# Kernel optimization log

Hardware: AMD Instinct MI355X
Metric: run time of the kernel (lower is better)

The kernel has to match this reference:

```python
import jax, jax.numpy as jnp
import numpy as np

B, T, E, H, O = 64, 512, 512, 512, 512

def setup_inputs() -> dict:
    key = jax.random.key(0)
    k1, k2, k3, k4, k5 = jax.random.split(key, 5)
    s1 = 1.0 / np.sqrt(E + H)
    s2 = 1.0 / np.sqrt(H)
    return {
        "x": jax.random.normal(k1, (B, T, E), dtype=jnp.float32),
        "W1": jax.random.uniform(k2, (H, E + H), dtype=jnp.float32, minval=-s1, maxval=s1),
        "b1": jax.random.uniform(k3, (H,), dtype=jnp.float32, minval=-s1, maxval=s1),
        "W2": jax.random.uniform(k4, (O, H), dtype=jnp.float32, minval=-s2, maxval=s2),
        "b2": jax.random.uniform(k5, (O,), dtype=jnp.float32, minval=-s2, maxval=s2),
    }

def reference(x, W1, b1, W2, b2):
    b = x.shape[0]
    h0 = jnp.zeros((b, x.shape[2]), dtype=x.dtype)

    def step(hidden, xt):
        inp = jnp.concatenate([xt, hidden], axis=1)          # [b, e+h]
        hidden = jax.nn.relu(inp @ W1.T + b1)                # [b, h]
        out = hidden @ W2.T + b2                             # [b, o]
        return hidden, out

    # scan over time: x -> [t, b, e]
    h_final, outs = jax.lax.scan(step, h0, jnp.swapaxes(x, 0, 1))
    return jnp.swapaxes(outs, 0, 1), h_final
```

## Files before the change

kernel.cpp:

```cpp
#include <hip/hip_runtime.h>
#include <cstddef>
#include <type_traits>

#define T_STEPS 512
#define BATCH   64
#define EDIM    512
#define HDIM    512
#define ODIM    512

#define W_ELEMS  (32 * 4 * 64 * 8)
#define HB_ELEMS (16 * 512)

typedef __bf16 bf16;
typedef __bf16 bf16x4 __attribute__((ext_vector_type(4)));
typedef __bf16 bf16x8 __attribute__((ext_vector_type(8)));
typedef float  f32x4  __attribute__((ext_vector_type(4)));

__device__ __forceinline__ void barrier_lds() {
  asm volatile("s_waitcnt lgkmcnt(0)\n\ts_barrier" ::: "memory");
  __builtin_amdgcn_sched_barrier(0);
}

__device__ __forceinline__ void gload_lds16(const bf16* g, bf16* l) {
  __builtin_amdgcn_global_load_lds(
      (const __attribute__((address_space(1))) unsigned int*)g,
      (__attribute__((address_space(3))) unsigned int*)l, 16, 0, 0);
}

__global__ __launch_bounds__(256) void conv_f32_bf16_kernel(
    const float* __restrict__ src, bf16* __restrict__ dst,
    int srow_stride, int drow_elems)
{
  size_t i = ((size_t)blockIdx.x * 256 + threadIdx.x) * 8;
  size_t row = i / drow_elems, col = i % drow_elems;
  const float* s = src + row * srow_stride + col;
  f32x4 a = *(const f32x4*)s;
  f32x4 b = *(const f32x4*)(s + 4);
  bf16x8 v;
#pragma unroll
  for (int u = 0; u < 4; ++u) { v[u] = (bf16)a[u]; v[u + 4] = (bf16)b[u]; }
  *(bf16x8*)(dst + i) = v;
}

template <typename XT, bool REMAP>
__global__ __launch_bounds__(256) void gemm_mfma_kernel(
    const XT* __restrict__ X, int ldx,
    const float* __restrict__ W, int ldw, int kw0,
    const float* __restrict__ bias,
    float* __restrict__ C, int ldc, int K)
{
  __shared__ __align__(16) bf16 Asm[8 * 64 * 8];
  __shared__ __align__(16) bf16 Bsm[8 * 64 * 8];

  const int tid  = threadIdx.x;
  const int row0 = blockIdx.x * 128;
  const int col0 = blockIdx.y * 128;
  const int w    = tid >> 6, lane = tid & 63;
  const int q    = lane >> 4, nl = lane & 15;
  const int wm   = w >> 1, wn = w & 1;

  const int srow = tid >> 2;
  const int sq   = tid & 3;
  f32x4 acc[4][4] = {};

  for (int k0 = 0; k0 < K; k0 += 32) {
#pragma unroll
    for (int rep = 0; rep < 2; ++rep) {
      int rl = srow + rep * 64;
      int mt = rl >> 4, snl = rl & 15;
      bf16x8 v;
      const XT* src = X + (size_t)(row0 + rl) * ldx + k0 + sq * 8;
      if constexpr (std::is_same_v<XT, float>) {
        f32x4 a0 = *(const f32x4*)src;
        f32x4 a1 = *(const f32x4*)(src + 4);
#pragma unroll
        for (int u = 0; u < 4; ++u) { v[u] = (bf16)a0[u]; v[u + 4] = (bf16)a1[u]; }
      } else {
        v = *(const bf16x8*)src;
      }
      *(bf16x8*)&Asm[(size_t)((mt * 4 + sq) * 16 + snl) * 8] = v;
    }
#pragma unroll
    for (int rep = 0; rep < 2; ++rep) {
      int rl = srow + rep * 64;
      int nt = rl >> 4, snl = rl & 15;
      const float* src = W + (size_t)(col0 + rl) * ldw + kw0 + k0 + sq * 8;
      f32x4 b0 = *(const f32x4*)src;
      f32x4 b1 = *(const f32x4*)(src + 4);
      bf16x8 v;
#pragma unroll
      for (int u = 0; u < 4; ++u) { v[u] = (bf16)b0[u]; v[u + 4] = (bf16)b1[u]; }
      *(bf16x8*)&Bsm[(size_t)((nt * 4 + sq) * 16 + snl) * 8] = v;
    }
    __syncthreads();

    bf16x8 a[4], b[4];
#pragma unroll
    for (int i = 0; i < 4; ++i)
      a[i] = *(bf16x8*)&Asm[(size_t)((wm * 4 + i) * 64 + lane) * 8];
#pragma unroll
    for (int j = 0; j < 4; ++j)
      b[j] = *(bf16x8*)&Bsm[(size_t)((wn * 4 + j) * 64 + lane) * 8];
#pragma unroll
    for (int i = 0; i < 4; ++i)
#pragma unroll
      for (int j = 0; j < 4; ++j)
        acc[i][j] = __builtin_amdgcn_mfma_f32_16x16x32_bf16(a[i], b[j], acc[i][j], 0, 0, 0);
    __syncthreads();
  }

#pragma unroll
  for (int i = 0; i < 4; ++i)
#pragma unroll
    for (int j = 0; j < 4; ++j) {
      int colg = col0 + wn * 64 + j * 16 + nl;
#pragma unroll
      for (int r = 0; r < 4; ++r) {
        size_t rowg = (size_t)(row0 + wm * 64 + i * 16 + q * 4 + r);
        size_t crow = REMAP ? (((rowg & (T_STEPS - 1)) << 6) | (rowg >> 9)) : rowg;
        C[crow * ldc + colg] = acc[i][j][r] + bias[colg];
      }
    }
}

template <bool REMAP>
__global__ __launch_bounds__(256) void gemm_lds_kernel(
    const bf16* __restrict__ Abf, int lda,
    const bf16* __restrict__ Bbf, int ldb,
    const float* __restrict__ bias,
    float* __restrict__ C, int ldc, int K)
{
  __shared__ __align__(16) bf16 Asm[8 * 64 * 8];
  __shared__ __align__(16) bf16 Bsm[8 * 64 * 8];

  const int tid  = threadIdx.x;
  const int row0 = blockIdx.x * 128;
  const int col0 = blockIdx.y * 128;
  const int w    = tid >> 6, lane = tid & 63;
  const int q    = lane >> 4, nl = lane & 15;
  const int wm   = w >> 1, wn = w & 1;

  f32x4 acc[4][4] = {};

  for (int k0 = 0; k0 < K; k0 += 32) {
#pragma unroll
    for (int rep = 0; rep < 2; ++rep) {
      int idx = tid + rep * 256;
      int mt = idx >> 6, sq = (idx >> 4) & 3, snl = idx & 15;
      const bf16* ga = Abf + (size_t)(row0 + mt * 16 + snl) * lda + k0 + sq * 8;
      gload_lds16(ga, Asm + (size_t)(rep * 4 + w) * 512);
      const bf16* gb = Bbf + (size_t)(col0 + mt * 16 + snl) * ldb + k0 + sq * 8;
      gload_lds16(gb, Bsm + (size_t)(rep * 4 + w) * 512);
    }
    __syncthreads();

    bf16x8 a[4], b[4];
#pragma unroll
    for (int i = 0; i < 4; ++i)
      a[i] = *(bf16x8*)&Asm[(size_t)((wm * 4 + i) * 64 + lane) * 8];
#pragma unroll
    for (int j = 0; j < 4; ++j)
      b[j] = *(bf16x8*)&Bsm[(size_t)((wn * 4 + j) * 64 + lane) * 8];
#pragma unroll
    for (int i = 0; i < 4; ++i)
#pragma unroll
      for (int j = 0; j < 4; ++j)
        acc[i][j] = __builtin_amdgcn_mfma_f32_16x16x32_bf16(a[i], b[j], acc[i][j], 0, 0, 0);
    __syncthreads();
  }

#pragma unroll
  for (int i = 0; i < 4; ++i)
#pragma unroll
    for (int j = 0; j < 4; ++j) {
      int colg = col0 + wn * 64 + j * 16 + nl;
#pragma unroll
      for (int r = 0; r < 4; ++r) {
        size_t rowg = (size_t)(row0 + wm * 64 + i * 16 + q * 4 + r);
        size_t crow = REMAP ? (((rowg & (T_STEPS - 1)) << 6) | (rowg >> 9)) : rowg;
        C[crow * ldc + colg] = acc[i][j][r] + bias[colg];
      }
    }
}

template <int DBUF>
__global__ __launch_bounds__(512, 2) void scan_kernel(
    const float* __restrict__ A,
    const float* __restrict__ W1,
    bf16* __restrict__ Hbf)
{
  extern __shared__ __align__(16) bf16 smem[];
  bf16* Wlds = smem;
  bf16* hb0  = smem + W_ELEMS;
  bf16* hb1  = DBUF ? (hb0 + HB_ELEMS) : hb0;

  const int tid  = threadIdx.x;
  const int c    = blockIdx.x;
  const int w    = tid >> 6, lane = tid & 63;
  const int q    = lane >> 4, nl = lane & 15;
  const int rb0  = c * 16;
  const int n0   = w * 64;
  const int sw   = (nl & 7) << 3;

  for (int idx = tid; idx < 32 * 4 * 64; idx += 512) {
    int l  = idx & 63;
    int kt = (idx >> 6) & 3;
    int tg = idx >> 8;
    int n  = tg * 16 + (l & 15);
    int k  = kt * 32 + (l >> 4) * 8;
    const float* src = W1 + (size_t)n * (EDIM + HDIM) + EDIM + k;
    bf16x8 v;
#pragma unroll
    for (int u = 0; u < 8; ++u) v[u] = (bf16)src[u];
    *(bf16x8*)&Wlds[(size_t)idx * 8] = v;
  }

  bf16x8 Wreg[4][12];
#pragma unroll
  for (int i = 0; i < 4; ++i) {
    int n = n0 + i * 16 + nl;
    const float* wrow = W1 + (size_t)n * (EDIM + HDIM) + EDIM;
#pragma unroll
    for (int kt2 = 0; kt2 < 12; ++kt2) {
      const float* src = wrow + (kt2 + 4) * 32 + q * 8;
      bf16x8 v;
#pragma unroll
      for (int u = 0; u < 8; ++u) v[u] = (bf16)src[u];
      Wreg[i][kt2] = v;
    }
  }
  __syncthreads();

  f32x4 An[4];
  {
    const float* ap = A + (size_t)(rb0 + nl) * HDIM + n0 + q * 4;
    An[0] = *(const f32x4*)(ap);
    An[1] = *(const f32x4*)(ap + 16);
    An[2] = *(const f32x4*)(ap + 32);
    An[3] = *(const f32x4*)(ap + 48);
  }

  f32x4 acc[4];

  for (int t = 0; t < T_STEPS; ++t) {
    bf16* hr = (t & 1) ? hb1 : hb0;
    bf16* hw = (t & 1) ? hb0 : hb1;

#pragma unroll
    for (int i = 0; i < 4; ++i) acc[i] = An[i];
    {
      int tn = (t + 1 < T_STEPS) ? t + 1 : 0;
      const float* ap = A + ((size_t)tn * BATCH + rb0 + nl) * HDIM + n0 + q * 4;
      An[0] = *(const f32x4*)(ap);
      An[1] = *(const f32x4*)(ap + 16);
      An[2] = *(const f32x4*)(ap + 32);
      An[3] = *(const f32x4*)(ap + 48);
    }

    if (t > 0) {
#pragma unroll
      for (int kt = 0; kt < 16; ++kt) {
        bf16x8 af = *(bf16x8*)&hr[nl * 512 + ((kt * 32 + q * 8) ^ sw)];
        if (kt < 4) {
#pragma unroll
          for (int i = 0; i < 4; ++i) {
            bf16x8 wb = *(bf16x8*)&Wlds[(size_t)(((w * 4 + i) * 4 + kt) * 64 + lane) * 8];
            acc[i] = __builtin_amdgcn_mfma_f32_16x16x32_bf16(wb, af, acc[i], 0, 0, 0);
          }
        } else {
#pragma unroll
          for (int i = 0; i < 4; ++i)
            acc[i] = __builtin_amdgcn_mfma_f32_16x16x32_bf16(Wreg[i][kt - 4], af, acc[i], 0, 0, 0);
        }
      }
    }

    if (!DBUF) barrier_lds();

#pragma unroll
    for (int i = 0; i < 4; ++i) {
      bf16x4 hv;
#pragma unroll
      for (int r = 0; r < 4; ++r) {
        float v = acc[i][r] > 0.0f ? acc[i][r] : 0.0f;
        hv[r] = (bf16)v;
      }
      *(bf16x4*)&hw[nl * 512 + ((n0 + i * 16 + q * 4) ^ sw)] = hv;
      *(bf16x4*)(Hbf + ((size_t)(rb0 + nl) * T_STEPS + t) * HDIM
                 + n0 + i * 16 + q * 4) = hv;
    }

    barrier_lds();
  }
}

__global__ __launch_bounds__(256) void copy_hfinal_kernel(
    const bf16* __restrict__ Hbf, float* __restrict__ out)
{
  int i = blockIdx.x * blockDim.x + threadIdx.x;
  int b = i / HDIM, n = i % HDIM;
  out[i] = (float)Hbf[((size_t)b * T_STEPS + (T_STEPS - 1)) * HDIM + n];
}

extern "C" void kernel_launch(void* const* d_in, const int* in_sizes, int n_in,
                              void* d_out, int out_size, void* d_ws, size_t ws_size,
                              hipStream_t stream) {
  const float* x  = (const float*)d_in[0];
  const float* W1 = (const float*)d_in[1];
  const float* b1 = (const float*)d_in[2];
  const float* W2 = (const float*)d_in[3];
  const float* b2 = (const float*)d_in[4];

  float* out = (float*)d_out;
  float* A   = out;

  bf16*  Hbf   = (bf16*)d_ws;
  size_t HBF_B = (size_t)BATCH * T_STEPS * HDIM * 2;
  bf16*  W1b   = (bf16*)((char*)d_ws + HBF_B);
  bf16*  W2b   = (bf16*)((char*)d_ws + HBF_B + 524288);
  bf16*  xbf   = (bf16*)((char*)d_ws + HBF_B + 1048576);
  const bool wok = ws_size >= HBF_B + 1048576;
  const bool xok = ws_size >= HBF_B + 1048576 + HBF_B;

  if (xok) {
    conv_f32_bf16_kernel<<<(BATCH * T_STEPS * EDIM) / 2048, 256, 0, stream>>>(
        x, xbf, EDIM, EDIM);
    conv_f32_bf16_kernel<<<(HDIM * EDIM) / 2048, 256, 0, stream>>>(
        W1, W1b, EDIM + HDIM, EDIM);
  }
  if (wok) {
    conv_f32_bf16_kernel<<<(ODIM * HDIM) / 2048, 256, 0, stream>>>(
        W2, W2b, HDIM, HDIM);
  }

  {
    dim3 grid(BATCH * T_STEPS / 128, HDIM / 128);
    if (xok)
      gemm_lds_kernel<true><<<grid, 256, 0, stream>>>(
          xbf, EDIM, W1b, EDIM, b1, A, HDIM, EDIM);
    else
      gemm_mfma_kernel<float, true><<<grid, 256, 0, stream>>>(
          x, EDIM, W1, EDIM + HDIM, 0, b1, A, HDIM, EDIM);
  }

  {
    int smem_dbuf = (W_ELEMS + 2 * HB_ELEMS) * 2;
    int smem_sbuf = (W_ELEMS + 1 * HB_ELEMS) * 2;
    hipError_t e = hipFuncSetAttribute(
        reinterpret_cast<const void*>(scan_kernel<1>),
        hipFuncAttributeMaxDynamicSharedMemorySize, smem_dbuf);
    if (e == hipSuccess) {
      scan_kernel<1><<<4, 512, smem_dbuf, stream>>>(A, W1, Hbf);
    } else {
      hipFuncSetAttribute(
          reinterpret_cast<const void*>(scan_kernel<0>),
          hipFuncAttributeMaxDynamicSharedMemorySize, smem_sbuf);
      scan_kernel<0><<<4, 512, smem_sbuf, stream>>>(A, W1, Hbf);
    }
  }

  {
    dim3 grid(BATCH * T_STEPS / 128, ODIM / 128);
    if (wok)
      gemm_lds_kernel<false><<<grid, 256, 0, stream>>>(
          Hbf, HDIM, W2b, HDIM, b2, out, ODIM, HDIM);
    else
      gemm_mfma_kernel<bf16, false><<<grid, 256, 0, stream>>>(
          Hbf, HDIM, W2, HDIM, 0, b2, out, ODIM, HDIM);
  }

  copy_hfinal_kernel<<<(BATCH * HDIM) / 256, 256, 0, stream>>>(
      Hbf, out + (size_t)BATCH * T_STEPS * ODIM);
}
```

Measured before the change: 1.384 ms.

## Overlap output GEMM with recurrent scan via cooperative kernel and progress flags

Fuses the sequential scan and the output projection GEMM into one cooperative launch. Four blocks run the recurrence and publish per-batch-group progress every 64 timesteps, while the remaining blocks spin-wait on those flags and compute output tiles as soon as their hidden states are ready. The aim is to hide the output GEMM behind the latency-bound scan. The input GEMM now uses the fp32 path, reading fp32 x directly without the bf16 conversion kernels, and it writes to a workspace buffer. This relies on co-residency and spin-wait correctness, and GEMM blocks sharing CUs with the scan blocks may slow the scan.

Result: no change. 1.383 ms (-0.1%).

```diff
diff --git a/kernel.cpp b/kernel.cpp
--- a/kernel.cpp
+++ b/kernel.cpp
@@ -10,6 +10,7 @@
 
 #define W_ELEMS  (32 * 4 * 64 * 8)
 #define HB_ELEMS (16 * 512)
+#define SMEM_COOP ((W_ELEMS + 2 * HB_ELEMS) * 2)
 
 typedef __bf16 bf16;
 typedef __bf16 bf16x4 __attribute__((ext_vector_type(4)));
@@ -123,79 +124,18 @@
     }
 }
 
-template <bool REMAP>
-__global__ __launch_bounds__(256) void gemm_lds_kernel(
-    const bf16* __restrict__ Abf, int lda,
-    const bf16* __restrict__ Bbf, int ldb,
-    const float* __restrict__ bias,
-    float* __restrict__ C, int ldc, int K)
-{
-  __shared__ __align__(16) bf16 Asm[8 * 64 * 8];
-  __shared__ __align__(16) bf16 Bsm[8 * 64 * 8];
-
-  const int tid  = threadIdx.x;
-  const int row0 = blockIdx.x * 128;
-  const int col0 = blockIdx.y * 128;
-  const int w    = tid >> 6, lane = tid & 63;
-  const int q    = lane >> 4, nl = lane & 15;
-  const int wm   = w >> 1, wn = w & 1;
-
-  f32x4 acc[4][4] = {};
-
-  for (int k0 = 0; k0 < K; k0 += 32) {
-#pragma unroll
-    for (int rep = 0; rep < 2; ++rep) {
-      int idx = tid + rep * 256;
-      int mt = idx >> 6, sq = (idx >> 4) & 3, snl = idx & 15;
-      const bf16* ga = Abf + (size_t)(row0 + mt * 16 + snl) * lda + k0 + sq * 8;
-      gload_lds16(ga, Asm + (size_t)(rep * 4 + w) * 512);
-      const bf16* gb = Bbf + (size_t)(col0 + mt * 16 + snl) * ldb + k0 + sq * 8;
-      gload_lds16(gb, Bsm + (size_t)(rep * 4 + w) * 512);
-    }
-    __syncthreads();
-
-    bf16x8 a[4], b[4];
-#pragma unroll
-    for (int i = 0; i < 4; ++i)
-      a[i] = *(bf16x8*)&Asm[(size_t)((wm * 4 + i) * 64 + lane) * 8];
-#pragma unroll
-    for (int j = 0; j < 4; ++j)
-      b[j] = *(bf16x8*)&Bsm[(size_t)((wn * 4 + j) * 64 + lane) * 8];
-#pragma unroll
-    for (int i = 0; i < 4; ++i)
-#pragma unroll
-      for (int j = 0; j < 4; ++j)
-        acc[i][j] = __builtin_amdgcn_mfma_f32_16x16x32_bf16(a[i], b[j], acc[i][j], 0, 0, 0);
-    __syncthreads();
-  }
-
-#pragma unroll
-  for (int i = 0; i < 4; ++i)
-#pragma unroll
-    for (int j = 0; j < 4; ++j) {
-      int colg = col0 + wn * 64 + j * 16 + nl;
-#pragma unroll
-      for (int r = 0; r < 4; ++r) {
-        size_t rowg = (size_t)(row0 + wm * 64 + i * 16 + q * 4 + r);
-        size_t crow = REMAP ? (((rowg & (T_STEPS - 1)) << 6) | (rowg >> 9)) : rowg;
-        C[crow * ldc + colg] = acc[i][j][r] + bias[colg];
-      }
-    }
-}
-
-template <int DBUF>
-__global__ __launch_bounds__(512, 2) void scan_kernel(
+template <int DBUF, bool PUB>
+__device__ __forceinline__ void scan_body(
     const float* __restrict__ A,
     const float* __restrict__ W1,
-    bf16* __restrict__ Hbf)
-{
-  extern __shared__ __align__(16) bf16 smem[];
+    bf16* __restrict__ Hbf,
+    bf16* smem, int c, int* prog)
+{
   bf16* Wlds = smem;
   bf16* hb0  = smem + W_ELEMS;
   bf16* hb1  = DBUF ? (hb0 + HB_ELEMS) : hb0;
 
   const int tid  = threadIdx.x;
-  const int c    = blockIdx.x;
   const int w    = tid >> 6, lane = tid & 63;
   const int q    = lane >> 4, nl = lane & 15;
   const int rb0  = c * 16;
@@ -291,6 +231,114 @@
     }
 
     barrier_lds();
+
+    if constexpr (PUB) {
+      if ((t & 63) == 63) {
+        asm volatile("s_waitcnt vmcnt(0)" ::: "memory");
+        __syncthreads();
+        if (tid == 0) {
+          __threadfence();
+          __hip_atomic_store(prog + c * 32, t + 1, __ATOMIC_RELAXED,
+                             __HIP_MEMORY_SCOPE_AGENT);
+        }
+      }
+    }
+  }
+}
+
+template <int DBUF>
+__global__ __launch_bounds__(512, 2) void scan_kernel(
+    const float* __restrict__ A, const float* __restrict__ W1,
+    bf16* __restrict__ Hbf)
+{
+  extern __shared__ __align__(16) bf16 smem[];
+  scan_body<DBUF, false>(A, W1, Hbf, smem, blockIdx.x, nullptr);
+}
+
+__global__ __launch_bounds__(512, 2) void coop_kernel(
+    const float* __restrict__ A, const float* __restrict__ W1,
+    bf16* __restrict__ Hbf, const bf16* __restrict__ W2b,
+    const float* __restrict__ b2, float* __restrict__ out,
+    int* __restrict__ progress)
+{
+  extern __shared__ __align__(16) bf16 smem[];
+  const int bid = blockIdx.x;
+  const int tid = threadIdx.x;
+
+  if (bid < 4) {
+    scan_body<1, true>(A, W1, Hbf, smem, bid, progress);
+    return;
+  }
+
+  bf16* Asm = smem;
+  bf16* Bsm = smem + 8 * 64 * 8;
+
+  const int wid  = bid - 4;
+  const bool act = tid < 256;
+  const int w    = (tid >> 6) & 3, lane = tid & 63;
+  const int q    = lane >> 4, nl = lane & 15;
+  const int wm   = w >> 1, wn = w & 1;
+
+  for (int g = wid; g < 1024; g += 252) {
+    int tc = g >> 8;
+    int b  = (g >> 2) & 63;
+    int by = g & 3;
+    int row0 = b * 512 + tc * 128;
+    int col0 = by * 128;
+    int need = tc * 128 + 128;
+
+    if (tid == 0) {
+      while (__hip_atomic_load(progress + (b >> 4) * 32, __ATOMIC_RELAXED,
+                               __HIP_MEMORY_SCOPE_AGENT) < need)
+        __builtin_amdgcn_s_sleep(8);
+      __threadfence();
+    }
+    __syncthreads();
+
+    f32x4 acc[4][4] = {};
+    for (int k0 = 0; k0 < HDIM; k0 += 32) {
+      if (act) {
+#pragma unroll
+        for (int rep = 0; rep < 2; ++rep) {
+          int idx = tid + rep * 256;
+          int mt = idx >> 6, sq = (idx >> 4) & 3, snl = idx & 15;
+          gload_lds16(Hbf + (size_t)(row0 + mt * 16 + snl) * HDIM + k0 + sq * 8,
+                      Asm + (size_t)(rep * 4 + w) * 512);
+          gload_lds16(W2b + (size_t)(col0 + mt * 16 + snl) * HDIM + k0 + sq * 8,
+                      Bsm + (size_t)(rep * 4 + w) * 512);
+        }
+      }
+      __syncthreads();
+      if (act) {
+        bf16x8 a[4], bb[4];
+#pragma unroll
+        for (int i = 0; i < 4; ++i)
+          a[i] = *(bf16x8*)&Asm[(size_t)((wm * 4 + i) * 64 + lane) * 8];
+#pragma unroll
+        for (int j = 0; j < 4; ++j)
+          bb[j] = *(bf16x8*)&Bsm[(size_t)((wn * 4 + j) * 64 + lane) * 8];
+#pragma unroll
+        for (int i = 0; i < 4; ++i)
+#pragma unroll
+          for (int j = 0; j < 4; ++j)
+            acc[i][j] = __builtin_amdgcn_mfma_f32_16x16x32_bf16(a[i], bb[j], acc[i][j], 0, 0, 0);
+      }
+      __syncthreads();
+    }
+
+    if (act) {
+#pragma unroll
+      for (int i = 0; i < 4; ++i)
+#pragma unroll
+        for (int j = 0; j < 4; ++j) {
+          int colg = col0 + wn * 64 + j * 16 + nl;
+#pragma unroll
+          for (int r = 0; r < 4; ++r) {
+            size_t rowg = (size_t)(row0 + wm * 64 + i * 16 + q * 4 + r);
+            out[rowg * ODIM + colg] = acc[i][j][r] + b2[colg];
+          }
+        }
+    }
   }
 }
 
@@ -312,61 +360,76 @@
   const float* b2 = (const float*)d_in[4];
 
   float* out = (float*)d_out;
-  float* A   = out;
 
   bf16*  Hbf   = (bf16*)d_ws;
   size_t HBF_B = (size_t)BATCH * T_STEPS * HDIM * 2;
-  bf16*  W1b   = (bf16*)((char*)d_ws + HBF_B);
-  bf16*  W2b   = (bf16*)((char*)d_ws + HBF_B + 524288);
-  bf16*  xbf   = (bf16*)((char*)d_ws + HBF_B + 1048576);
-  const bool wok = ws_size >= HBF_B + 1048576;
-  const bool xok = ws_size >= HBF_B + 1048576 + HBF_B;
-
-  if (xok) {
-    conv_f32_bf16_kernel<<<(BATCH * T_STEPS * EDIM) / 2048, 256, 0, stream>>>(
-        x, xbf, EDIM, EDIM);
-    conv_f32_bf16_kernel<<<(HDIM * EDIM) / 2048, 256, 0, stream>>>(
-        W1, W1b, EDIM + HDIM, EDIM);
-  }
-  if (wok) {
+  size_t OFF_W2B = HBF_B;
+  size_t OFF_A   = HBF_B + 524288;
+  size_t OFF_FLG = OFF_A + (size_t)BATCH * T_STEPS * HDIM * 4;
+  size_t NEED    = OFF_FLG + 4096;
+
+  bf16*  W2b  = (bf16*)((char*)d_ws + OFF_W2B);
+  float* Aws  = (float*)((char*)d_ws + OFF_A);
+  int*   prog = (int*)((char*)d_ws + OFF_FLG);
+
+  int smem_dbuf = SMEM_COOP;
+  int smem_sbuf = (W_ELEMS + 1 * HB_ELEMS) * 2;
+
+  bool coop_ok = ws_size >= NEED;
+  if (coop_ok)
+    coop_ok = hipFuncSetAttribute(
+                  reinterpret_cast<const void*>(coop_kernel),
+                  hipFuncAttributeMaxDynamicSharedMemorySize, SMEM_COOP)
+              == hipSuccess;
+  if (coop_ok) {
+    int mb = 0;
+    if (hipOccupancyMaxActiveBlocksPerMultiprocessor(
+            &mb, reinterpret_cast<const void*>(coop_kernel), 512,
+            (size_t)SMEM_COOP) != hipSuccess)
+      mb = 0;
+    coop_ok = (mb >= 1);
+  }
+
+  if (coop_ok) {
+    hipMemsetAsync(prog, 0, 4096, stream);
     conv_f32_bf16_kernel<<<(ODIM * HDIM) / 2048, 256, 0, stream>>>(
         W2, W2b, HDIM, HDIM);
-  }
-
-  {
-    dim3 grid(BATCH * T_STEPS / 128, HDIM / 128);
-    if (xok)
-      gemm_lds_kernel<true><<<grid, 256, 0, stream>>>(
-          xbf, EDIM, W1b, EDIM, b1, A, HDIM, EDIM);
-    else
-      gemm_mfma_kernel<float, true><<<grid, 256, 0, stream>>>(
-          x, EDIM, W1, EDIM + HDIM, 0, b1, A, HDIM, EDIM);
-  }
-
-  {
-    int smem_dbuf = (W_ELEMS + 2 * HB_ELEMS) * 2;
-    int smem_sbuf = (W_ELEMS + 1 * HB_ELEMS) * 2;
+    dim3 g1(BATCH * T_STEPS / 128, HDIM / 128);
+    gemm_mfma_kernel<float, true><<<g1, 256, 0, stream>>>(
+        x, EDIM, W1, EDIM + HDIM, 0, b1, Aws, HDIM, EDIM);
+    const float* Ac  = Aws;  const float* W1c = W1;  bf16* Hc = Hbf;
+    const bf16*  W2c = W2b;  const float* b2c = b2;  float* oc = out;
+    int* pc = prog;
+    void* kargs[] = {&Ac, &W1c, &Hc, &W2c, &b2c, &oc, &pc};
+    hipError_t ce = hipLaunchCooperativeKernel(
+        reinterpret_cast<const void*>(coop_kernel), dim3(256), dim3(512),
+        kargs, (unsigned)SMEM_COOP, stream);
+    if (ce != hipSuccess) {
+      hipFuncSetAttribute(reinterpret_cast<const void*>(scan_kernel<1>),
+                          hipFuncAttributeMaxDynamicSharedMemorySize, smem_dbuf);
+      scan_kernel<1><<<4, 512, smem_dbuf, stream>>>(Aws, W1, Hbf);
+      dim3 g3(BATCH * T_STEPS / 128, ODIM / 128);
+      gemm_mfma_kernel<bf16, false><<<g3, 256, 0, stream>>>(
+          Hbf, HDIM, W2, HDIM, 0, b2, out, ODIM, HDIM);
+    }
+  } else {
+    float* A = out;
+    dim3 g1(BATCH * T_STEPS / 128, HDIM / 128);
+    gemm_mfma_kernel<float, true><<<g1, 256, 0, stream>>>(
+        x, EDIM, W1, EDIM + HDIM, 0, b1, A, HDIM, EDIM);
     hipError_t e = hipFuncSetAttribute(
         reinterpret_cast<const void*>(scan_kernel<1>),
         hipFuncAttributeMaxDynamicSharedMemorySize, smem_dbuf);
     if (e == hipSuccess) {
       scan_kernel<1><<<4, 512, smem_dbuf, stream>>>(A, W1, Hbf);
     } else {
-      hipFuncSetAttribute(
-          reinterpret_cast<const void*>(scan_kernel<0>),
-          hipFuncAttributeMaxDynamicSharedMemorySize, smem_sbuf);
+      hipFuncSetAttribute(reinterpret_cast<const void*>(scan_kernel<0>),
+                          hipFuncAttributeMaxDynamicSharedMemorySize, smem_sbuf);
       scan_kernel<0><<<4, 512, smem_sbuf, stream>>>(A, W1, Hbf);
     }
-  }
-
-  {
-    dim3 grid(BATCH * T_STEPS / 128, ODIM / 128);
-    if (wok)
-      gemm_lds_kernel<false><<<grid, 256, 0, stream>>>(
-          Hbf, HDIM, W2b, HDIM, b2, out, ODIM, HDIM);
-    else
-      gemm_mfma_kernel<bf16, false><<<grid, 256, 0, stream>>>(
-          Hbf, HDIM, W2, HDIM, 0, b2, out, ODIM, HDIM);
+    dim3 g3(BATCH * T_STEPS / 128, ODIM / 128);
+    gemm_mfma_kernel<bf16, false><<<g3, 256, 0, stream>>>(
+        Hbf, HDIM, W2, HDIM, 0, b2, out, ODIM, HDIM);
   }
 
   copy_hfinal_kernel<<<(BATCH * HDIM) / 256, 256, 0, stream>>>(
```
